# Kernel tuning notes

Measured on AMD Instinct MI355X. Metric: run time of the kernel, lower is better.

## Reference

```python
import jax, jax.numpy as jnp
import numpy as np

DT = 0.02
STEPS = 50          # SDE_MAX_T / SDE_DT
S = 16              # SDE_N_SIM
TEMP = 20.0
DETACH_K = 10
LATENT = 128
B = 16384


def setup_inputs() -> dict:
    key = jax.random.key(0)
    ks = jax.random.split(key, 8)
    z = jax.random.normal(ks[0], (B, LATENT), jnp.float32)
    W1 = jax.random.normal(ks[1], (64, LATENT + 2), jnp.float32) / np.sqrt(LATENT + 2)
    b1 = jnp.zeros((64,), jnp.float32)
    W2 = jax.random.normal(ks[2], (2, 64), jnp.float32) / np.sqrt(64)
    b2 = jnp.array([0.5, 0.0], jnp.float32)  # matches nn.init in _init_sde
    Wb = jax.random.normal(ks[3], (1, LATENT), jnp.float32) / np.sqrt(LATENT)
    bb = jnp.zeros((1,), jnp.float32)
    Wn = jax.random.normal(ks[4], (1, LATENT), jnp.float32) / np.sqrt(LATENT)
    bn = jnp.zeros((1,), jnp.float32)
    out_scale = jnp.array([0.001, 0.001, 0.1], jnp.float32)
    out_bias = jnp.zeros((3,), jnp.float32)
    noise = jax.random.normal(ks[5], (STEPS, B, S), jnp.float32)
    return {"z": z, "W1": W1, "b1": b1, "W2": W2, "b2": b2, "Wb": Wb, "bb": bb,
            "Wn": Wn, "bn": bn, "out_scale": out_scale, "out_bias": out_bias,
            "noise": noise}


def reference(z, W1, b1, W2, b2, Wb, bb, Wn, bn, out_scale, out_bias, noise):
    sqrt_dt = DT ** 0.5
    boundary = jax.nn.softplus(z @ Wb.T + bb)[:, 0] + 0.3   # (B,)
    ndt = jax.nn.softplus(z @ Wn.T + bn)[:, 0] + 0.05       # (B,)
    half_b = boundary * 0.5
    Bn = z.shape[0]
    z_exp = jnp.broadcast_to(z[:, None, :], (Bn, S, z.shape[1]))  # (B,S,L)

    def step(carry, xs):
        x, log_surv, exp_rt, exp_corr = carry
        k, nz = xs
        # periodic detach of the state (no-op for forward values)
        x = jnp.where((k > 0) & (k % DETACH_K == 0), jax.lax.stop_gradient(x), x)
        t_val = k.astype(x.dtype) * DT
        t_col = jnp.broadcast_to(t_val, x.shape)[..., None]          # (B,S,1)
        inp = jnp.concatenate([x[..., None], t_col, z_exp], axis=-1)  # (B,S,L+2)
        h = jnp.tanh(inp @ W1.T + b1)
        dyn = h @ W2.T + b2                                           # (B,S,2)
        drift = jnp.clip(dyn[..., 0], -5.0, 5.0)
        diff = jax.nn.softplus(dyn[..., 1]) + 0.1
        x = jnp.clip(x + drift * DT + diff * sqrt_dt * nz, -10.0, 10.0)
        dist = jnp.abs(x) - half_b[:, None]
        hazard = jnp.clip(jax.nn.sigmoid(TEMP * dist), 0.0, 0.99)
        surv_before = jnp.exp(jnp.maximum(log_surv, -50.0))
        cross_p = surv_before * hazard
        log_surv = log_surv + jnp.log1p(-hazard)
        t_now = (k + 1).astype(x.dtype) * DT
        exp_rt = exp_rt + cross_p * t_now
        exp_corr = exp_corr + cross_p * (x > 0).astype(x.dtype)
        return (x, log_surv, exp_rt, exp_corr), None

    zero = jnp.zeros((Bn, S), z.dtype)
    carry0 = (zero, zero, zero, zero)
    (x, log_surv, exp_rt, exp_corr), _ = jax.lax.scan(
        step, carry0, (jnp.arange(STEPS), noise))

    remaining = jnp.exp(jnp.maximum(log_surv, -50.0))
    exp_rt = exp_rt + remaining * (STEPS * DT)
    exp_corr = exp_corr + remaining * 0.5
    rt_ms = (exp_rt + ndt[:, None]) * 1000.0
    raw = jnp.stack([rt_ms.mean(axis=1),
                     rt_ms.std(axis=1, ddof=1) + 0.001,   # torch unbiased std
                     exp_corr.mean(axis=1)], axis=1)
    out = raw * out_scale + out_bias
    return jnp.nan_to_num(out, nan=0.0)
```

## Files before the change

### kernel.cpp

```cpp
#include <hip/hip_runtime.h>
#include <hip/hip_fp16.h>
#include <math.h>

#define SDE_B 16384
#define SDE_S 16
#define SDE_STEPS 50
#define SDE_L 128
#define SDE_DT 0.02f
#define SDE_SQRT_DT 0.14142135623730951f
#define SDE_TEMP 20.0f
#define LOG2E 1.44269504088896340736f
#define LN2 0.69314718055994530942f
#define SC2 (2.0f * LOG2E)
#define CT (SDE_TEMP * LOG2E)

typedef float f32x2 __attribute__((ext_vector_type(2)));

#if __has_builtin(__builtin_amdgcn_exp2f)
__device__ __forceinline__ float fexp2(float x) { return __builtin_amdgcn_exp2f(x); }
#else
__device__ __forceinline__ float fexp2(float x) { return __exp2f(x); }
#endif

#if __has_builtin(__builtin_amdgcn_logf)
__device__ __forceinline__ float flog2(float x) { return __builtin_amdgcn_logf(x); }
#else
__device__ __forceinline__ float flog2(float x) { return __log2f(x); }
#endif

#if __has_builtin(__builtin_amdgcn_rcpf)
__device__ __forceinline__ float frcp(float x) { return __builtin_amdgcn_rcpf(x); }
#else
__device__ __forceinline__ float frcp(float x) { return 1.0f / x; }
#endif

#if __has_builtin(__builtin_amdgcn_fmed3f)
__device__ __forceinline__ float fmed3(float x, float lo, float hi) {
    return __builtin_amdgcn_fmed3f(x, lo, hi);
}
#else
__device__ __forceinline__ float fmed3(float x, float lo, float hi) {
    return fminf(fmaxf(x, lo), hi);
}
#endif

__device__ __forceinline__ float uni(float v) {
#if __has_builtin(__builtin_amdgcn_readfirstlane)
    return __int_as_float(__builtin_amdgcn_readfirstlane(__float_as_int(v)));
#else
    return v;
#endif
}

__device__ __forceinline__ float softplus_fast(float y) {
    float m = fmaxf(y, 0.0f);
    float e = fexp2(-fabsf(y) * LOG2E);
    return fmaf(LN2, flog2(1.0f + e), m);
}

template <int CTL>
__device__ __forceinline__ float dpp_qp(float v) {
#if __has_builtin(__builtin_amdgcn_mov_dpp)
    return __int_as_float(__builtin_amdgcn_mov_dpp(__float_as_int(v), CTL, 0xF, 0xF, true));
#else
    return v;
#endif
}

__device__ __forceinline__ f32x2 quad_sum2(f32x2 v) {
#if __has_builtin(__builtin_amdgcn_mov_dpp)
    f32x2 w;
    w.x = dpp_qp<0xB1>(v.x); w.y = dpp_qp<0xB1>(v.y);
    v += w;
    w.x = dpp_qp<0x4E>(v.x); w.y = dpp_qp<0x4E>(v.y);
    v += w;
    return v;
#else
    v.x += __shfl_xor(v.x, 1, 64); v.y += __shfl_xor(v.y, 1, 64);
    v.x += __shfl_xor(v.x, 2, 64); v.y += __shfl_xor(v.y, 2, 64);
    return v;
#endif
}

__device__ __forceinline__ float fixnum(float v) {
    if (isnan(v)) return 0.0f;
    if (isinf(v)) return v > 0.0f ? 3.4028234663852886e38f : -3.4028234663852886e38f;
    return v;
}

__global__ void __launch_bounds__(256, 2) sde_kernel(
    const float* __restrict__ z,  const float* __restrict__ W1,
    const float* __restrict__ b1, const float* __restrict__ W2,
    const float* __restrict__ b2, const float* __restrict__ Wb,
    const float* __restrict__ bb, const float* __restrict__ Wn,
    const float* __restrict__ bn, const float* __restrict__ osc,
    const float* __restrict__ obias, const float* __restrict__ noise,
    float* __restrict__ out)
{
    const int lane = threadIdx.x & 63;
    const int wv = threadIdx.x >> 6;
    const int b = blockIdx.x * 4 + wv;
    const int s = lane >> 2;
    const int q = lane & 3;

    const float* zr = z + (size_t)b * SDE_L;

    float accz = b1[lane];
    {
        const float* wrow = W1 + lane * 130 + 2;
        #pragma unroll
        for (int m = 0; m < SDE_L; m += 2) {
            float2 w = *(const float2*)(wrow + m);
            accz = fmaf(zr[m], w.x, accz);
            accz = fmaf(zr[m + 1], w.y, accz);
        }
    }
    accz *= SC2;

    float zb0 = zr[2 * lane], zb1 = zr[2 * lane + 1];
    float pb = fmaf(zb0, Wb[2 * lane], zb1 * Wb[2 * lane + 1]);
    float pn = fmaf(zb0, Wn[2 * lane], zb1 * Wn[2 * lane + 1]);
    #pragma unroll
    for (int off = 32; off > 0; off >>= 1) {
        pb += __shfl_xor(pb, off, 64);
        pn += __shfl_xor(pn, off, 64);
    }
    const float Hh = uni(CT * (0.5f * (softplus_fast(pb + bb[0]) + 0.3f)));
    const float ndt = uni(softplus_fast(pn + bn[0]) + 0.05f);

    f32x2 zw2[8], wx2[8], wt2[8], wa2[8], wb2[8];
    float S2a = 0.0f, S2b = 0.0f;
    #pragma unroll
    for (int p = 0; p < 8; ++p) {
        int j0 = 4 * (2 * p) + q, j1 = 4 * (2 * p + 1) + q;
        zw2[p].x = __shfl(accz, j0, 64);
        zw2[p].y = __shfl(accz, j1, 64);
        float2 wa0 = *(const float2*)(W1 + j0 * 130);
        float2 wa1 = *(const float2*)(W1 + j1 * 130);
        wx2[p].x = wa0.x * SC2; wx2[p].y = wa1.x * SC2;
        wt2[p].x = wa0.y * SC2; wt2[p].y = wa1.y * SC2;
        float a0w = W2[j0], a1w = W2[j1];
        float b0w = W2[64 + j0], b1w = W2[64 + j1];
        S2a += a0w + a1w;
        S2b += b0w + b1w;
        wa2[p].x = -2.0f * a0w; wa2[p].y = -2.0f * a1w;
        wb2[p].x = -2.0f * b0w; wb2[p].y = -2.0f * b1w;
    }
    const float a0base = fmaf(0.25f, b2[0], S2a);
    const float a1base = fmaf(0.25f, b2[1], S2b);

    const int noff = b * SDE_S + s;

    float x = 0.0f, surv = 1.0f, ert = 0.0f, ecs = 0.0f;
    float t = 0.0f;
    const f32x2 one2 = {1.0f, 1.0f};
    float nz_cur = noise[noff];

    for (int k = 0; k < SDE_STEPS; ++k) {
        int kn = (k + 1 < SDE_STEPS) ? k + 1 : k;
        float nz_nxt = noise[kn * (SDE_B * SDE_S) + noff];

        f32x2 acc0 = {0.0f, 0.0f}, acc1 = {0.0f, 0.0f};
        #pragma unroll
        for (int p = 0; p < 8; ++p) {
            f32x2 pr = x * wx2[p] + (t * wt2[p] + zw2[p]);
            f32x2 e; e.x = fexp2(pr.x); e.y = fexp2(pr.y);
            f32x2 d = e + one2;
            f32x2 g; g.x = frcp(d.x); g.y = frcp(d.y);
            acc0 += g * wa2[p];
            acc1 += g * wb2[p];
        }
        f32x2 ab;
        ab.x = a0base + (acc0.x + acc0.y);
        ab.y = a1base + (acc1.x + acc1.y);
        ab = quad_sum2(ab);
        float drift = fmed3(ab.x, -5.0f, 5.0f);
        float sp = softplus_fast(ab.y);
        float diffs = fmaf(sp, SDE_SQRT_DT, 0.1f * SDE_SQRT_DT);
        x = fmaf(drift, SDE_DT, fmaf(diffs, nz_cur, x));
        x = fmed3(x, -10.0f, 10.0f);
        float e = fexp2(fmaf(fabsf(x), -CT, Hh));
        float hz = fminf(frcp(1.0f + e), 0.99f);
        float cross = surv * hz;
        surv = surv - cross;
        t += SDE_DT;
        ert = fmaf(cross, t, ert);
        ecs += __builtin_copysignf(cross, x);
        nz_cur = nz_nxt;
    }

    ert += surv;
    float corr = (1.0f + ecs) * 0.5f;
    float rt = ert + ndt;

    float sr = (q == 0) ? rt : 0.0f;
    float scr = (q == 0) ? corr : 0.0f;
    #pragma unroll
    for (int off = 32; off > 0; off >>= 1) {
        sr += __shfl_xor(sr, off, 64);
        scr += __shfl_xor(scr, off, 64);
    }
    float mean = sr * (1.0f / 16.0f);
    float d = rt - mean;
    float vv = (q == 0) ? d * d : 0.0f;
    #pragma unroll
    for (int off = 32; off > 0; off >>= 1) vv += __shfl_xor(vv, off, 64);

    if (lane == 0) {
        float std_ms = sqrtf(vv * (1.0f / 15.0f)) * 1000.0f + 0.001f;
        float o0 = fmaf(mean * 1000.0f, osc[0], obias[0]);
        float o1 = fmaf(std_ms, osc[1], obias[1]);
        float o2 = fmaf(scr * (1.0f / 16.0f), osc[2], obias[2]);
        out[b * 3 + 0] = fixnum(o0);
        out[b * 3 + 1] = fixnum(o1);
        out[b * 3 + 2] = fixnum(o2);
    }
}

extern "C" void kernel_launch(void* const* d_in, const int* in_sizes, int n_in,
                              void* d_out, int out_size, void* d_ws, size_t ws_size,
                              hipStream_t stream) {
    const float* z     = (const float*)d_in[0];
    const float* W1    = (const float*)d_in[1];
    const float* b1    = (const float*)d_in[2];
    const float* W2    = (const float*)d_in[3];
    const float* b2    = (const float*)d_in[4];
    const float* Wb    = (const float*)d_in[5];
    const float* bb    = (const float*)d_in[6];
    const float* Wn    = (const float*)d_in[7];
    const float* bn    = (const float*)d_in[8];
    const float* osc   = (const float*)d_in[9];
    const float* obias = (const float*)d_in[10];
    const float* noise = (const float*)d_in[11];
    float* out = (float*)d_out;

    dim3 grid(SDE_B / 4), block(256);
    sde_kernel<<<grid, block, 0, stream>>>(z, W1, b1, W2, b2, Wb, bb, Wn, bn,
                                           osc, obias, noise, out);
}
```

Before: 317.6 us.

## Split hidden units across eight lanes with two waves per batch row

Each batch row is now handled by a 128-thread block of two waves, each wave covering 8 simulations. The 64 hidden units are split across 8 lanes instead of 4, so each lane evaluates 8 tanh units per step instead of 16. The lane-group reduction gains a third DPP stage (row half-mirror), and the final mean/std statistics are combined through shared memory with a block barrier. This shortens the per-step serial dependency chain at the cost of doubling the total lane count, duplicating the z projection prologue and per-simulation scalar work across more lanes, and adding one extra reduction step per iteration.

```diff
diff --git a/kernel.cpp b/kernel.cpp
--- a/kernel.cpp
+++ b/kernel.cpp
@@ -59,7 +59,7 @@
 }
 
 template <int CTL>
-__device__ __forceinline__ float dpp_qp(float v) {
+__device__ __forceinline__ float dpp_mv(float v) {
 #if __has_builtin(__builtin_amdgcn_mov_dpp)
     return __int_as_float(__builtin_amdgcn_mov_dpp(__float_as_int(v), CTL, 0xF, 0xF, true));
 #else
@@ -67,17 +67,20 @@
 #endif
 }
 
-__device__ __forceinline__ f32x2 quad_sum2(f32x2 v) {
+__device__ __forceinline__ f32x2 oct_sum2(f32x2 v) {
 #if __has_builtin(__builtin_amdgcn_mov_dpp)
     f32x2 w;
-    w.x = dpp_qp<0xB1>(v.x); w.y = dpp_qp<0xB1>(v.y);
+    w.x = dpp_mv<0xB1>(v.x);  w.y = dpp_mv<0xB1>(v.y);
     v += w;
-    w.x = dpp_qp<0x4E>(v.x); w.y = dpp_qp<0x4E>(v.y);
+    w.x = dpp_mv<0x4E>(v.x);  w.y = dpp_mv<0x4E>(v.y);
+    v += w;
+    w.x = dpp_mv<0x141>(v.x); w.y = dpp_mv<0x141>(v.y);
     v += w;
     return v;
 #else
     v.x += __shfl_xor(v.x, 1, 64); v.y += __shfl_xor(v.y, 1, 64);
     v.x += __shfl_xor(v.x, 2, 64); v.y += __shfl_xor(v.y, 2, 64);
+    v.x += __shfl_xor(v.x, 4, 64); v.y += __shfl_xor(v.y, 4, 64);
     return v;
 #endif
 }
@@ -88,7 +91,7 @@
     return v;
 }
 
-__global__ void __launch_bounds__(256, 2) sde_kernel(
+__global__ void __launch_bounds__(128) sde_kernel(
     const float* __restrict__ z,  const float* __restrict__ W1,
     const float* __restrict__ b1, const float* __restrict__ W2,
     const float* __restrict__ b2, const float* __restrict__ Wb,
@@ -99,9 +102,9 @@
 {
     const int lane = threadIdx.x & 63;
     const int wv = threadIdx.x >> 6;
-    const int b = blockIdx.x * 4 + wv;
-    const int s = lane >> 2;
-    const int q = lane & 3;
+    const int b = blockIdx.x;
+    const int s = lane >> 3;
+    const int q = lane & 7;
 
     const float* zr = z + (size_t)b * SDE_L;
 
@@ -128,11 +131,11 @@
     const float Hh = uni(CT * (0.5f * (softplus_fast(pb + bb[0]) + 0.3f)));
     const float ndt = uni(softplus_fast(pn + bn[0]) + 0.05f);
 
-    f32x2 zw2[8], wx2[8], wt2[8], wa2[8], wb2[8];
+    f32x2 zw2[4], wx2[4], wt2[4], wa2[4], wb2[4];
     float S2a = 0.0f, S2b = 0.0f;
     #pragma unroll
-    for (int p = 0; p < 8; ++p) {
-        int j0 = 4 * (2 * p) + q, j1 = 4 * (2 * p + 1) + q;
+    for (int p = 0; p < 4; ++p) {
+        int j0 = 16 * p + q, j1 = 16 * p + 8 + q;
         zw2[p].x = __shfl(accz, j0, 64);
         zw2[p].y = __shfl(accz, j1, 64);
         float2 wa0 = *(const float2*)(W1 + j0 * 130);
@@ -146,10 +149,10 @@
         wa2[p].x = -2.0f * a0w; wa2[p].y = -2.0f * a1w;
         wb2[p].x = -2.0f * b0w; wb2[p].y = -2.0f * b1w;
     }
-    const float a0base = fmaf(0.25f, b2[0], S2a);
-    const float a1base = fmaf(0.25f, b2[1], S2b);
-
-    const int noff = b * SDE_S + s;
+    const float a0base = fmaf(0.125f, b2[0], S2a);
+    const float a1base = fmaf(0.125f, b2[1], S2b);
+
+    const int noff = b * SDE_S + (wv * 8 + s);
 
     float x = 0.0f, surv = 1.0f, ert = 0.0f, ecs = 0.0f;
     float t = 0.0f;
@@ -160,9 +163,10 @@
         int kn = (k + 1 < SDE_STEPS) ? k + 1 : k;
         float nz_nxt = noise[kn * (SDE_B * SDE_S) + noff];
 
-        f32x2 acc0 = {0.0f, 0.0f}, acc1 = {0.0f, 0.0f};
-        #pragma unroll
-        for (int p = 0; p < 8; ++p) {
+        f32x2 acc0; acc0.x = a0base; acc0.y = 0.0f;
+        f32x2 acc1; acc1.x = a1base; acc1.y = 0.0f;
+        #pragma unroll
+        for (int p = 0; p < 4; ++p) {
             f32x2 pr = x * wx2[p] + (t * wt2[p] + zw2[p]);
             f32x2 e; e.x = fexp2(pr.x); e.y = fexp2(pr.y);
             f32x2 d = e + one2;
@@ -171,9 +175,9 @@
             acc1 += g * wb2[p];
         }
         f32x2 ab;
-        ab.x = a0base + (acc0.x + acc0.y);
-        ab.y = a1base + (acc1.x + acc1.y);
-        ab = quad_sum2(ab);
+        ab.x = acc0.x + acc0.y;
+        ab.y = acc1.x + acc1.y;
+        ab = oct_sum2(ab);
         float drift = fmed3(ab.x, -5.0f, 5.0f);
         float sp = softplus_fast(ab.y);
         float diffs = fmaf(sp, SDE_SQRT_DT, 0.1f * SDE_SQRT_DT);
@@ -193,27 +197,36 @@
     float corr = (1.0f + ecs) * 0.5f;
     float rt = ert + ndt;
 
-    float sr = (q == 0) ? rt : 0.0f;
-    float scr = (q == 0) ? corr : 0.0f;
-    #pragma unroll
-    for (int off = 32; off > 0; off >>= 1) {
-        sr += __shfl_xor(sr, off, 64);
-        scr += __shfl_xor(scr, off, 64);
-    }
-    float mean = sr * (1.0f / 16.0f);
-    float d = rt - mean;
-    float vv = (q == 0) ? d * d : 0.0f;
-    #pragma unroll
-    for (int off = 32; off > 0; off >>= 1) vv += __shfl_xor(vv, off, 64);
-
-    if (lane == 0) {
-        float std_ms = sqrtf(vv * (1.0f / 15.0f)) * 1000.0f + 0.001f;
-        float o0 = fmaf(mean * 1000.0f, osc[0], obias[0]);
-        float o1 = fmaf(std_ms, osc[1], obias[1]);
-        float o2 = fmaf(scr * (1.0f / 16.0f), osc[2], obias[2]);
-        out[b * 3 + 0] = fixnum(o0);
-        out[b * 3 + 1] = fixnum(o1);
-        out[b * 3 + 2] = fixnum(o2);
+    __shared__ float rt_lds[SDE_S], cr_lds[SDE_S];
+    if (q == 0) {
+        rt_lds[wv * 8 + s] = rt;
+        cr_lds[wv * 8 + s] = corr;
+    }
+    __syncthreads();
+    if (wv == 0) {
+        float rtv = (lane < 16) ? rt_lds[lane] : 0.0f;
+        float cv  = (lane < 16) ? cr_lds[lane] : 0.0f;
+        float sr = rtv, scr = cv;
+        #pragma unroll
+        for (int off = 8; off > 0; off >>= 1) {
+            sr += __shfl_xor(sr, off, 64);
+            scr += __shfl_xor(scr, off, 64);
+        }
+        float mean = sr * (1.0f / 16.0f);
+        float d = rtv - mean;
+        float vv = (lane < 16) ? d * d : 0.0f;
+        #pragma unroll
+        for (int off = 8; off > 0; off >>= 1) vv += __shfl_xor(vv, off, 64);
+
+        if (lane == 0) {
+            float std_ms = sqrtf(vv * (1.0f / 15.0f)) * 1000.0f + 0.001f;
+            float o0 = fmaf(mean * 1000.0f, osc[0], obias[0]);
+            float o1 = fmaf(std_ms, osc[1], obias[1]);
+            float o2 = fmaf(scr * (1.0f / 16.0f), osc[2], obias[2]);
+            out[b * 3 + 0] = fixnum(o0);
+            out[b * 3 + 1] = fixnum(o1);
+            out[b * 3 + 2] = fixnum(o2);
+        }
     }
 }
 
@@ -234,7 +247,7 @@
     const float* noise = (const float*)d_in[11];
     float* out = (float*)d_out;
 
-    dim3 grid(SDE_B / 4), block(256);
+    dim3 grid(SDE_B), block(128);
     sde_kernel<<<grid, block, 0, stream>>>(z, W1, b1, W2, b2, Wb, bb, Wn, bn,
                                            osc, obias, noise, out);
 }
```

Result: slower. 372.5 us (+17.3%).
